# Kernel optimization log

Hardware: AMD Instinct MI355X
Metric: run time of the kernel (lower is better)

The kernel has to match this reference:

```python
import jax, jax.numpy as jnp
import numpy as np

NUM_HEADS, KEY_DIM, BLOCK, HALO = 8, 64, 8, 4
KV_KERNEL = BLOCK + 2 * HALO  # 16
EMB = NUM_HEADS * KEY_DIM     # 512


def setup_inputs() -> dict:
    key = jax.random.key(0)
    k = jax.random.split(key, 6)
    stddev = KEY_DIM ** -0.5
    return {
        "x": jax.random.normal(k[0], (8, 64, 64, 512), jnp.float32),
        "wq": jax.random.normal(k[1], (512, EMB), jnp.float32) * 0.02,
        "wkv": jax.random.normal(k[2], (512, 2 * EMB), jnp.float32) * 0.02,
        "wout": jax.random.normal(k[3], (EMB, EMB), jnp.float32) * 0.02,
        "pos_w": jax.random.normal(k[4], (KEY_DIM, 2 * KV_KERNEL - 1), jnp.float32) * stddev,
        "pos_h": jax.random.normal(k[5], (KEY_DIM, 2 * KV_KERNEL - 1), jnp.float32) * stddev,
    }


def rel_to_abs(rel):
    # rel: [B, N, hh, ww, 2*pos_dim-1] -> [B, N, hh, ww, pos_dim]
    b, n, hh, ww, dim = rel.shape
    pos_dim = (dim + 1) // 2
    gap = pos_dim - ww
    flat = rel.reshape(b, n, hh, ww * dim)[:, :, :, ww - 1:-1]
    return flat.reshape(b, n, hh, ww, 2 * (pos_dim - 1))[:, :, :, :, gap:pos_dim + gap]


def halo_forward(x, wq, wkv, wout, pos_w, pos_h):
    B, H, W, C = x.shape
    h, w = H // BLOCK, W // BLOCK
    K = KV_KERNEL
    scale = 1.0 / jnp.sqrt(jnp.asarray(KEY_DIM, x.dtype))

    # Query: [B, hd, h, w, block^2, key_dim]
    q = (x @ wq) * scale
    q = q.reshape(B, h, BLOCK, w, BLOCK, NUM_HEADS, KEY_DIM)
    attn_q = q.transpose(0, 5, 1, 3, 2, 4, 6).reshape(B, NUM_HEADS, h, w, BLOCK * BLOCK, KEY_DIM)

    # Overlapping halo KV windows (im2col-style gather, like tf.image.extract_patches)
    kv = x @ wkv
    kv_p = jnp.pad(kv, ((0, 0), (HALO, HALO), (HALO, HALO), (0, 0)))
    idx_h = jnp.arange(h)[:, None] * BLOCK + jnp.arange(K)[None, :]  # [h, K]
    idx_w = jnp.arange(w)[:, None] * BLOCK + jnp.arange(K)[None, :]  # [w, K]
    patches = kv_p[:, idx_h][:, :, :, idx_w]          # [B, h, K, w, K, 2*EMB]
    patches = patches.transpose(0, 1, 3, 2, 4, 5)     # [B, h, w, K, K, 2*EMB]
    patches = patches.reshape(B, h, w, K * K, NUM_HEADS, 2 * KEY_DIM)
    patches = patches.transpose(0, 4, 1, 2, 3, 5)     # [B, hd, h, w, K^2, 2*key_dim]
    key_t, val = patches[..., :KEY_DIM], patches[..., KEY_DIM:]

    scores = jnp.einsum('bnhwqc,bnhwkc->bnhwqk', attn_q, key_t)  # [B,hd,h,w,bq,bk]

    # Relative position logits (width + height), query already carries qk_scale
    pos_q = attn_q.reshape(B, NUM_HEADS * h * w, BLOCK, BLOCK, KEY_DIM)
    rel_w = rel_to_abs(pos_q @ pos_w)                                      # [B,N,hb,wb,K]
    rel_h = rel_to_abs(pos_q.transpose(0, 1, 3, 2, 4) @ pos_h)
    rel_h = rel_h.transpose(0, 1, 3, 2, 4)                                 # [B,N,hb,wb,K]
    pos = rel_w[..., None, :] + rel_h[..., :, None]                        # [B,N,hb,wb,Kh,Kw]
    pos = pos.reshape(B, NUM_HEADS, h, w, BLOCK * BLOCK, K * K)

    attn = jax.nn.softmax(scores + pos, axis=-1)
    out = jnp.einsum('bnhwqk,bnhwkc->bnhwqc', attn, val)
    out = out.reshape(B, NUM_HEADS, h, w, BLOCK, BLOCK, KEY_DIM)
    out = out.transpose(0, 2, 4, 3, 5, 1, 6).reshape(B, H, W, EMB)
    return out @ wout


def reference(x, wq, wkv, wout, pos_w, pos_h):
    return halo_forward(x, wq, wkv, wout, pos_w, pos_h)
```

## Files before the change

### kernel.cpp

```cpp
#include <hip/hip_runtime.h>
#include <hip/hip_fp16.h>
#include <math.h>

typedef _Float16 f16x8 __attribute__((ext_vector_type(8)));
typedef _Float16 f16x4 __attribute__((ext_vector_type(4)));
typedef float    f32x4 __attribute__((ext_vector_type(4)));

#define M_TOT 32768
#define VROW  4608
#define LOG2E 1.44269504088896f

__device__ __forceinline__ void gload16(const void* g, void* l) {
    __builtin_amdgcn_global_load_lds(
        (const __attribute__((address_space(1))) unsigned int*)g,
        (__attribute__((address_space(3))) unsigned int*)l, 16, 0, 0);
}

__device__ __forceinline__ f32x4 mfma32(f16x8 a, f16x8 b, f32x4 c) {
    return __builtin_amdgcn_mfma_f32_16x16x32_f16(a, b, c, 0, 0, 0);
}

__global__ __launch_bounds__(256) void prep(
    const float* __restrict__ wq, const float* __restrict__ wkv,
    const float* __restrict__ wout,
    const float* __restrict__ posw, const float* __restrict__ posh,
    __half* __restrict__ wT, __half* __restrict__ woT,
    __half* __restrict__ posT, __half* __restrict__ vTp, __half* __restrict__ zp)
{
    const int bid = blockIdx.x, t = threadIdx.x;
    if (bid < 4096) {
        const int id = bid * 256 + t;
        const int nr = id >> 9, k = id & 511;
        if (nr < 512) {
            wT[(size_t)nr * 512 + k] = __float2half(wq[k * 512 + nr] * (0.125f * LOG2E));
        } else if (nr < 1536) {
            wT[(size_t)nr * 512 + k] = __float2half(wkv[k * 1024 + (nr - 512)]);
        } else {
            woT[(size_t)(nr - 1536) * 512 + k] = __float2half(wout[k * 512 + (nr - 1536)]);
        }
    } else if (bid < 6144) {
        const int id = (bid - 4096) * 256 + t;
        const int row = id >> 7, rem = id & 127;
        const int y = rem >> 1, side = rem & 1;
        f16x4 z = {(_Float16)0.f, (_Float16)0.f, (_Float16)0.f, (_Float16)0.f};
        *(f16x4*)(vTp + (size_t)row * VROW + y * 72 + side * 68) = z;
    } else if (bid < 6160) {
        const int id = (bid - 6144) * 256 + t;
        const int tb = id >> 11, idx = (id >> 6) & 31, d = id & 63;
        const float* src = tb ? posh : posw;
        posT[id] = __float2half((idx < 31) ? src[d * 31 + idx] : 0.f);
    } else {
        if (t < 16) {
            float4 z = make_float4(0.f, 0.f, 0.f, 0.f);
            *(float4*)(zp + t * 8) = z;
        }
    }
}

template <int MODE, int NBN>
__global__ __launch_bounds__(256) void mfma_gemm(
    const void* __restrict__ A, const __half* __restrict__ Bt,
    __half* __restrict__ q16, __half* __restrict__ k16, __half* __restrict__ vTp,
    float* __restrict__ outf)
{
    __shared__ __align__(16) char As[128 * 128];
    __shared__ __align__(16) char Bs[128 * 128];

    const int t = threadIdx.x;
    const int l = t & 63, w = t >> 6;
    const int wr = w >> 1, wc = w & 1;
    const int lr = l & 15, hi = l >> 4;

    const int bid = blockIdx.x;
    const int xcd = bid & 7, loc = bid >> 3;
    const int half = loc / (16 * NBN);
    const int rem  = loc % (16 * NBN);
    const int bn   = rem >> 4;
    const int bm   = xcd * 32 + half * 16 + (rem & 15);

    const float*  Af = (const float*)A;
    const __half* Ah = (const __half*)A;

    f32x4 acc[4][4];
    #pragma unroll
    for (int i = 0; i < 4; ++i)
        #pragma unroll
        for (int j = 0; j < 4; ++j) acc[i][j] = (f32x4){0.f, 0.f, 0.f, 0.f};

    const int sch = (t & 7);

    for (int k0 = 0; k0 < 512; k0 += 64) {
        if (MODE == 0) {
            #pragma unroll
            for (int it = 0; it < 4; ++it) {
                const int row = it * 32 + (t >> 3);
                const float4* src = (const float4*)(Af + (size_t)(bm * 128 + row) * 512 + k0 + sch * 8);
                const float4 f0 = src[0];
                const float4 f1 = src[1];
                __half2 hh[4];
                hh[0] = __floats2half2_rn(f0.x, f0.y);
                hh[1] = __floats2half2_rn(f0.z, f0.w);
                hh[2] = __floats2half2_rn(f1.x, f1.y);
                hh[3] = __floats2half2_rn(f1.z, f1.w);
                *(float4*)(As + row * 128 + ((sch ^ (row & 7)) * 16)) = *(float4*)hh;
            }
        } else {
            #pragma unroll
            for (int it = 0; it < 4; ++it) {
                const int row = it * 32 + (t >> 3);
                const int kk  = k0 + ((sch ^ (row & 7)) * 8);
                gload16(Ah + (size_t)(bm * 128 + row) * 512 + kk,
                        As + (it * 256 + w * 64) * 16);
            }
        }
        #pragma unroll
        for (int it = 0; it < 4; ++it) {
            const int row = it * 32 + (t >> 3);
            const int kk  = k0 + ((sch ^ (row & 7)) * 8);
            gload16(Bt + (size_t)(bn * 128 + row) * 512 + kk,
                    Bs + (it * 256 + w * 64) * 16);
        }
        __syncthreads();

        #pragma unroll
        for (int dc = 0; dc < 2; ++dc) {
            f16x8 af[4], bf[4];
            #pragma unroll
            for (int i = 0; i < 4; ++i) {
                const int ra = wr * 64 + i * 16 + lr;
                af[i] = *(const f16x8*)(As + ra * 128 + (((dc * 4 + hi) ^ (ra & 7)) * 16));
            }
            #pragma unroll
            for (int j = 0; j < 4; ++j) {
                const int rb = wc * 64 + j * 16 + lr;
                bf[j] = *(const f16x8*)(Bs + rb * 128 + (((dc * 4 + hi) ^ (rb & 7)) * 16));
            }
            #pragma unroll
            for (int i = 0; i < 4; ++i)
                #pragma unroll
                for (int j = 0; j < 4; ++j)
                    acc[i][j] = mfma32(af[i], bf[j], acc[i][j]);
        }
        __syncthreads();
    }

    const int lq = hi;
    #pragma unroll
    for (int i = 0; i < 4; ++i) {
        #pragma unroll
        for (int j = 0; j < 4; ++j) {
            const int row0 = bm * 128 + wr * 64 + i * 16 + lq * 4;
            const int col  = bn * 128 + wc * 64 + j * 16 + lr;
            if (MODE == 1) {
                #pragma unroll
                for (int r = 0; r < 4; ++r)
                    outf[(size_t)(row0 + r) * 512 + col] = acc[i][j][r];
            } else if (bn < 4) {
                #pragma unroll
                for (int r = 0; r < 4; ++r)
                    q16[(size_t)(row0 + r) * 512 + col] = __float2half(acc[i][j][r]);
            } else if (wc == 0) {
                const int head = bn - 4, d2 = j * 16 + lr;
                #pragma unroll
                for (int r = 0; r < 4; ++r)
                    k16[(size_t)(row0 + r) * 512 + head * 64 + d2] = __float2half(acc[i][j][r]);
            } else {
                const int head = bn - 4, d2 = j * 16 + lr;
                const int bb = row0 >> 12, pix = row0 & 4095;
                const int py = pix >> 6, px = pix & 63;
                f16x4 pv;
                #pragma unroll
                for (int r = 0; r < 4; ++r) pv[r] = (_Float16)acc[i][j][r];
                *(f16x4*)(vTp + ((size_t)((bb * 8 + head) * 64 + d2)) * VROW + py * 72 + px + 4) = pv;
            }
        }
    }
}

__global__ __launch_bounds__(256, 4) void halo_attn(
    const __half* __restrict__ qbuf, const __half* __restrict__ kbuf,
    const __half* __restrict__ vTp, const __half* __restrict__ posT,
    const __half* __restrict__ zp, __half* __restrict__ obuf)
{
    __shared__ __align__(16) char KP[64 * 520];
    __shared__ __align__(16) char POSB[6336];
    __shared__ float red[4][64];

    __half* RW = (__half*)POSB;
    __half* RH = (__half*)(POSB + 3168);
    float (*red2)[64] = (float(*)[64])POSB;

    const int hw = blockIdx.x;
    const int wg = (hw & 7) * 512 + (hw >> 3);
    const int wb = wg & 7, hb = (wg >> 3) & 7, n = (wg >> 6) & 7, b = wg >> 9;
    const int t = threadIdx.x;
    const int l = t & 63, g = t >> 6;
    const int hi = l >> 4, c15 = l & 15;

    #pragma unroll
    for (int it = 0; it < 8; ++it) {
        const int cid = it * 256 + t;
        const int S = cid * 16;
        const int row = S >> 7;
        const int d0h = (((S & 127) >> 4) ^ (row & 7)) * 8;
        const int ky = hb * 8 - 4 + (row >> 4);
        const int kx = wb * 8 - 4 + (row & 15);
        const bool ok = ((unsigned)ky < 64u) && ((unsigned)kx < 64u);
        const __half* src = ok ? (kbuf + ((size_t)((b * 64 + ky) * 64 + kx)) * 512 + n * 64 + d0h)
                               : zp;
        gload16(src, KP + (it * 256 + g * 64) * 16);
    }

    f16x8 vfrag[8];
    {
        const __half* vrow = vTp + ((size_t)((b * 8 + n) * 64 + g * 16 + c15)) * VROW;
        const int xoff = wb * 8 + (hi & 1) * 8;
        #pragma unroll
        for (int kc = 0; kc < 8; ++kc) {
            const int ki = kc * 2 + (hi >> 1);
            const int y = hb * 8 - 4 + ki;
            const __half* p = ((unsigned)y < 64u) ? (vrow + y * 72 + xoff) : zp;
            vfrag[kc] = *(const f16x8*)p;
        }
    }

    f16x8 qreg[4][2];
    #pragma unroll
    for (int qf = 0; qf < 4; ++qf) {
        const int q = qf * 16 + c15;
        const size_t pix = (size_t)((b * 64 + hb * 8 + (q >> 3)) * 64 + wb * 8 + (q & 7));
        #pragma unroll
        for (int dc = 0; dc < 2; ++dc)
            qreg[qf][dc] = *(const f16x8*)(qbuf + pix * 512 + n * 64 + dc * 32 + hi * 8);
    }

    {
        const int tb = g >> 1, ih = g & 1;
        f32x4 accp[4];
        #pragma unroll
        for (int qf = 0; qf < 4; ++qf) accp[qf] = (f32x4){0.f, 0.f, 0.f, 0.f};
        #pragma unroll
        for (int dc = 0; dc < 2; ++dc) {
            const f16x8 a = *(const f16x8*)(posT + tb * 2048 + (ih * 16 + c15) * 64 + dc * 32 + hi * 8);
            #pragma unroll
            for (int qf = 0; qf < 4; ++qf)
                accp[qf] = mfma32(a, qreg[qf][dc], accp[qf]);
        }
        __half* dst = tb ? RH : RW;
        #pragma unroll
        for (int qf = 0; qf < 4; ++qf)
            #pragma unroll
            for (int r = 0; r < 4; ++r) {
                const unsigned idx8 = (unsigned)(ih * 16 + hi * 4 + r) - 8u;
                if (idx8 < 23u)
                    dst[idx8 * 66 + qf * 16 + c15] = __float2half(accp[qf][r]);
            }
    }
    __syncthreads();

    f32x4 accs[4][4];
    #pragma unroll
    for (int kf = 0; kf < 4; ++kf)
        #pragma unroll
        for (int qf = 0; qf < 4; ++qf) accs[kf][qf] = (f32x4){0.f, 0.f, 0.f, 0.f};

    __builtin_amdgcn_s_setprio(1);
    #pragma unroll
    for (int kf = 0; kf < 4; ++kf) {
        const int row = g * 64 + kf * 16 + c15;
        #pragma unroll
        for (int dc = 0; dc < 2; ++dc) {
            const int off = (row * 128 + dc * 64 + hi * 16) ^ ((row & 7) << 4);
            f16x8 a = *(const f16x8*)(KP + off);
            #pragma unroll
            for (int qf = 0; qf < 4; ++qf)
                accs[kf][qf] = mfma32(a, qreg[qf][dc], accs[kf][qf]);
        }
    }
    __builtin_amdgcn_s_setprio(0);

    float mq[4];
    #pragma unroll
    for (int qf = 0; qf < 4; ++qf) {
        const int q = qf * 16 + c15;
        const int qj = q & 7, qi = q >> 3;
        float pa[4], pb[4];
        #pragma unroll
        for (int r = 0; r < 4; ++r)  pa[r] = __half2float(RW[(hi * 4 + r + 7 - qj) * 66 + q]);
        #pragma unroll
        for (int kf = 0; kf < 4; ++kf) pb[kf] = __half2float(RH[(g * 4 + kf + 7 - qi) * 66 + q]);
        float mm = -1e30f;
        #pragma unroll
        for (int kf = 0; kf < 4; ++kf)
            #pragma unroll
            for (int r = 0; r < 4; ++r) {
                const float s = accs[kf][qf][r] + pa[r] + pb[kf];
                accs[kf][qf][r] = s;
                mm = fmaxf(mm, s);
            }
        mm = fmaxf(mm, __shfl_xor(mm, 16));
        mm = fmaxf(mm, __shfl_xor(mm, 32));
        mq[qf] = mm;
    }
    if (l < 16) {
        #pragma unroll
        for (int qf = 0; qf < 4; ++qf) red[g][qf * 16 + l] = mq[qf];
    }
    __syncthreads();

    float sums[4];
    #pragma unroll
    for (int qf = 0; qf < 4; ++qf) {
        const int q = qf * 16 + c15;
        const float mfull = fmaxf(fmaxf(red[0][q], red[1][q]), fmaxf(red[2][q], red[3][q]));
        float ss = 0.f;
        #pragma unroll
        for (int kf = 0; kf < 4; ++kf)
            #pragma unroll
            for (int r = 0; r < 4; ++r) {
                const float p = exp2f(accs[kf][qf][r] - mfull);
                accs[kf][qf][r] = p;
                ss += p;
            }
        ss += __shfl_xor(ss, 16);
        ss += __shfl_xor(ss, 32);
        sums[qf] = ss;
        #pragma unroll
        for (int kf = 0; kf < 4; ++kf) {
            __half2 h01 = __floats2half2_rn(accs[kf][qf][0], accs[kf][qf][1]);
            __half2 h23 = __floats2half2_rn(accs[kf][qf][2], accs[kf][qf][3]);
            uint2 wv;
            wv.x = *(unsigned*)&h01;
            wv.y = *(unsigned*)&h23;
            *(uint2*)(KP + q * 520 + (g * 64 + kf * 16 + hi * 4) * 2) = wv;
        }
    }
    if (l < 16) {
        #pragma unroll
        for (int qf = 0; qf < 4; ++qf) red2[g][qf * 16 + l] = sums[qf];
    }
    __syncthreads();

    f32x4 acco[4];
    #pragma unroll
    for (int qf = 0; qf < 4; ++qf) acco[qf] = (f32x4){0.f, 0.f, 0.f, 0.f};
    __builtin_amdgcn_s_setprio(1);
    #pragma unroll
    for (int kc = 0; kc < 8; ++kc) {
        const f16x8 bf = vfrag[kc];
        #pragma unroll
        for (int qf = 0; qf < 4; ++qf) {
            const char* pp = KP + (qf * 16 + c15) * 520 + kc * 64 + hi * 16;
            const f16x4 p0 = *(const f16x4*)pp;
            const f16x4 p1 = *(const f16x4*)(pp + 8);
            const f16x8 af = __builtin_shufflevector(p0, p1, 0, 1, 2, 3, 4, 5, 6, 7);
            acco[qf] = mfma32(af, bf, acco[qf]);
        }
    }
    __builtin_amdgcn_s_setprio(0);

    #pragma unroll
    for (int qf = 0; qf < 4; ++qf) {
        #pragma unroll
        for (int r = 0; r < 4; ++r) {
            const int q = qf * 16 + hi * 4 + r;
            const float den = red2[0][q] + red2[1][q] + red2[2][q] + red2[3][q];
            const float v = acco[qf][r] * __builtin_amdgcn_rcpf(den);
            const size_t pix = (size_t)((b * 64 + hb * 8 + (q >> 3)) * 64 + wb * 8 + (q & 7));
            obuf[pix * 512 + n * 64 + g * 16 + c15] = __float2half(v);
        }
    }
}

extern "C" void kernel_launch(void* const* d_in, const int* in_sizes, int n_in,
                              void* d_out, int out_size, void* d_ws, size_t ws_size,
                              hipStream_t stream)
{
    const float* x    = (const float*)d_in[0];
    const float* wq   = (const float*)d_in[1];
    const float* wkv  = (const float*)d_in[2];
    const float* wout = (const float*)d_in[3];
    const float* posw = (const float*)d_in[4];
    const float* posh = (const float*)d_in[5];
    float* out = (float*)d_out;

    const size_t NPIX = (size_t)M_TOT * 512;
    const size_t NVTP = (size_t)64 * 64 * VROW;
    __half* wT   = (__half*)d_ws;
    __half* woT  = wT + (size_t)1536 * 512;
    __half* q16  = woT + (size_t)512 * 512;
    __half* k16  = q16 + NPIX;
    __half* vTp  = k16 + NPIX;
    __half* o16  = vTp + NVTP;
    __half* zp   = o16 + NPIX;
    __half* posT = zp + 128;

    prep<<<6161, 256, 0, stream>>>(wq, wkv, wout, posw, posh,
                                   wT, woT, posT, vTp, zp);

    mfma_gemm<0, 12><<<3072, 256, 0, stream>>>(x, wT, q16, k16, vTp, nullptr);

    halo_attn<<<4096, 256, 0, stream>>>(q16, k16, vTp, posT, zp, o16);

    mfma_gemm<1, 4><<<1024, 256, 0, stream>>>(o16, woT, nullptr, nullptr, nullptr, out);
}
```

Measured before the change: 212.7 us.

## Load fp32 A tiles directly to LDS and convert to fp16 at fragment read

In the fp32-input GEMM mode, the A tile is now staged into LDS as raw fp32 through async global_load_lds with a 16-way XOR swizzle, replacing register loads followed by conversion and LDS stores. The fp32-to-fp16 conversion moves to the point where each wave reads its MFMA fragments, which doubles A's LDS footprint to 32KB in that mode and repeats the conversion once per consuming wave. The block-to-tile mapping is also simplified to a plain bm/bn split per XCD, which changes L2 reuse ordering.

```diff
diff --git a/kernel.cpp b/kernel.cpp
--- a/kernel.cpp
+++ b/kernel.cpp
@@ -63,8 +63,8 @@
     __half* __restrict__ q16, __half* __restrict__ k16, __half* __restrict__ vTp,
     float* __restrict__ outf)
 {
-    __shared__ __align__(16) char As[128 * 128];
-    __shared__ __align__(16) char Bs[128 * 128];
+    __shared__ __align__(16) char As[(MODE == 0) ? 32768 : 16384];
+    __shared__ __align__(16) char Bs[16384];
 
     const int t = threadIdx.x;
     const int l = t & 63, w = t >> 6;
@@ -73,10 +73,8 @@
 
     const int bid = blockIdx.x;
     const int xcd = bid & 7, loc = bid >> 3;
-    const int half = loc / (16 * NBN);
-    const int rem  = loc % (16 * NBN);
-    const int bn   = rem >> 4;
-    const int bm   = xcd * 32 + half * 16 + (rem & 15);
+    const int bm  = xcd * 32 + (loc & 31);
+    const int bn  = loc >> 5;
 
     const float*  Af = (const float*)A;
     const __half* Ah = (const __half*)A;
@@ -92,17 +90,11 @@
     for (int k0 = 0; k0 < 512; k0 += 64) {
         if (MODE == 0) {
             #pragma unroll
-            for (int it = 0; it < 4; ++it) {
-                const int row = it * 32 + (t >> 3);
-                const float4* src = (const float4*)(Af + (size_t)(bm * 128 + row) * 512 + k0 + sch * 8);
-                const float4 f0 = src[0];
-                const float4 f1 = src[1];
-                __half2 hh[4];
-                hh[0] = __floats2half2_rn(f0.x, f0.y);
-                hh[1] = __floats2half2_rn(f0.z, f0.w);
-                hh[2] = __floats2half2_rn(f1.x, f1.y);
-                hh[3] = __floats2half2_rn(f1.z, f1.w);
-                *(float4*)(As + row * 128 + ((sch ^ (row & 7)) * 16)) = *(float4*)hh;
+            for (int it = 0; it < 8; ++it) {
+                const int cid = it * 256 + t;
+                const int row = cid >> 4, c = cid & 15;
+                gload16(Af + (size_t)(bm * 128 + row) * 512 + k0 + ((c ^ (row & 15)) << 2),
+                        As + (it * 256 + w * 64) * 16);
             }
         } else {
             #pragma unroll
@@ -128,7 +120,22 @@
             #pragma unroll
             for (int i = 0; i < 4; ++i) {
                 const int ra = wr * 64 + i * 16 + lr;
-                af[i] = *(const f16x8*)(As + ra * 128 + (((dc * 4 + hi) ^ (ra & 7)) * 16));
+                if (MODE == 0) {
+                    const int s  = ra & 15;
+                    const int c0 = dc * 8 + hi * 2;
+                    const int pA = ra * 256 + ((c0 ^ s) << 4);
+                    const int pB = ra * 256 + (((c0 ^ s) ^ 1) << 4);
+                    const float4 fA = *(const float4*)(As + pA);
+                    const float4 fB = *(const float4*)(As + pB);
+                    __half2 hh[4];
+                    hh[0] = __floats2half2_rn(fA.x, fA.y);
+                    hh[1] = __floats2half2_rn(fA.z, fA.w);
+                    hh[2] = __floats2half2_rn(fB.x, fB.y);
+                    hh[3] = __floats2half2_rn(fB.z, fB.w);
+                    af[i] = *(f16x8*)hh;
+                } else {
+                    af[i] = *(const f16x8*)(As + ra * 128 + (((dc * 4 + hi) ^ (ra & 7)) * 16));
+                }
             }
             #pragma unroll
             for (int j = 0; j < 4; ++j) {
```

New measurement: 223.4 us. +5.0%, slower.
